# Kernel tuning notes

Hardware: AMD Instinct MI355X
Metric: run time of the kernel (lower is better)

## Reference

```python
import jax, jax.numpy as jnp
import numpy as np

B, M, N, I, O, NM = 16, 256, 256, 64, 64, 16


def setup_inputs() -> dict:
    key = jax.random.key(0)
    k1, k2, k3, k4, k5 = jax.random.split(key, 5)
    glorot = 1.0 / np.sqrt(I + O)
    return {
        "x": jax.random.normal(k1, (B, M, N, I), dtype=jnp.float32),
        "fw1": jax.random.normal(k2, (I, O, NM, NM, 2), dtype=jnp.float32) * glorot,
        "fw2": jax.random.normal(k3, (I, O, NM, NM, 2), dtype=jnp.float32) * glorot,
        "W": jax.random.normal(k4, (I, O), dtype=jnp.float32) * glorot,
        "b": jnp.zeros((O,), dtype=jnp.float32),
    }


def reference(x, fw1, fw2, W, b):
    # x: [B, M, N, I] -> [B, I, M, N]
    Bs, Ms, Ns, Is = x.shape
    nm = fw1.shape[2]
    xt = jnp.transpose(x, (0, 3, 1, 2))
    # forward rFFT over spatial dims, scaled by 1/sqrt(M*N) as in the TF code
    x_ft = jnp.fft.rfft2(xt, s=(Ms, Ns))  # [B, I, M, N//2+1] complex64
    x_ft = x_ft / jnp.asarray(np.sqrt(Ms * Ns), dtype=x_ft.dtype)
    # complex weights (stack-of-2 real/imag -> complex); complex einsum is
    # exactly the real/imag stacked matmul in the original
    w1 = jax.lax.complex(fw1[..., 0], fw1[..., 1])
    w2 = jax.lax.complex(fw2[..., 0], fw2[..., 1])
    top = jnp.einsum('bixy,ioxy->boxy', x_ft[:, :, :nm, :nm], w1)
    bot = jnp.einsum('bixy,ioxy->boxy', x_ft[:, :, -nm:, :nm], w2)
    mid = jnp.zeros((Bs, top.shape[1], Ms - 2 * nm, nm), dtype=top.dtype)
    out_ft = jnp.concatenate([top, mid, bot], axis=2)          # [B, O, M, nm]
    pad = jnp.zeros((Bs, top.shape[1], Ms, Ms // 2 + 1 - nm), dtype=top.dtype)
    out_ft = jnp.concatenate([out_ft, pad], axis=3)            # [B, O, M, M//2+1]
    y = jnp.fft.irfft2(out_ft, s=(Ns, Ms))                     # [B, O, N, M]
    # TF rescale: sqrt(prod of last two dims of out_ft) = sqrt(N*(M//2+1))
    y = y * jnp.asarray(np.sqrt(Ns * (Ms // 2 + 1)), dtype=y.dtype)
    y = jnp.transpose(y, (0, 2, 3, 1))                         # [B, M, N, O]
    return jax.nn.relu(y @ W + b + y)
```

## Files before the change

kernel.cpp:

```cpp
#include <hip/hip_runtime.h>
#include <hip/hip_bf16.h>


#define PI2F 6.283185307179586f

typedef __attribute__((ext_vector_type(8))) short short8v;
typedef __attribute__((ext_vector_type(4))) float f32x4;

static __device__ __forceinline__ unsigned short f_to_bf16(float f) {
  unsigned int u = __float_as_uint(f);
  u += 0x7fffu + ((u >> 16) & 1u);
  return (unsigned short)(u >> 16);
}
static __device__ __forceinline__ unsigned int pack_bf16(float lo, float hi) {
  return (unsigned int)f_to_bf16(lo) | ((unsigned int)f_to_bf16(hi) << 16);
}

__global__ __launch_bounds__(256) void k_prep(const float* __restrict__ fw1,
                                              const float* __restrict__ fw2,
                                              unsigned int* __restrict__ wTb,
                                              unsigned short* __restrict__ Eg,
                                              unsigned short* __restrict__ CSg,
                                              const float* __restrict__ Wg,
                                              unsigned short* __restrict__ Wtb) {
  int t = threadIdx.x;
  if (blockIdx.x == 256) {
    const float SC = 1.0f / 256.0f;
#pragma unroll
    for (int ky = 0; ky < 16; ++ky) {
      int idx = (ky * t) & 255;
      float ss, cc;
      sincosf(PI2F * (float)idx * (1.0f / 256.0f), &ss, &cc);
      Eg[(2 * ky) * 256 + t]     = f_to_bf16(cc * SC);
      Eg[(2 * ky + 1) * 256 + t] = f_to_bf16(-ss * SC);
      CSg[t * 32 + 2 * ky]       = f_to_bf16(cc);
      CSg[t * 32 + 2 * ky + 1]   = f_to_bf16(ss);
    }
#pragma unroll
    for (int k = 0; k < 16; ++k) {
      int p = k * 256 + t;
      Wtb[(p & 63) * 64 + (p >> 6)] = f_to_bf16(Wg[p]);
    }
    return;
  }
  int a  = blockIdx.x >> 3;
  int ic = blockIdx.x & 7;
  const float* w = (a < 16) ? fw1 : fw2;
  int xx = a & 15;
#pragma unroll
  for (int k = 0; k < 2; ++k) {
    int p = k * 256 + t;
    int i = ic * 8 + (p >> 6);
    int o = p & 63;
    const float4* s4 = reinterpret_cast<const float4*>(
        w + ((((size_t)i * 64 + o) * 16 + xx) * 16) * 2);
#pragma unroll
    for (int j = 0; j < 8; ++j) {
      float4 q = s4[j];
      wTb[(((size_t)(2 * j) * 32 + a) * 64 + i) * 64 + o]     = pack_bf16(q.x, q.y);
      wTb[(((size_t)(2 * j + 1) * 32 + a) * 64 + i) * 64 + o] = pack_bf16(q.z, q.w);
    }
  }
}

__global__ __launch_bounds__(256) void k1_mfma(const float* __restrict__ x,
                                               const unsigned short* __restrict__ Eg,
                                               unsigned int* __restrict__ Tb) {
  __shared__ __align__(16) unsigned short El[32 * 264];
  __shared__ __align__(16) float xs[2][2048];
  int bm = blockIdx.x;
  int b = bm >> 8, m = bm & 255;
  int tid = threadIdx.x;

  {
    const unsigned int* src = reinterpret_cast<const unsigned int*>(Eg);
    unsigned int* dst = reinterpret_cast<unsigned int*>(El);
#pragma unroll
    for (int t = 0; t < 16; ++t) {
      int idx = t * 256 + tid;
      dst[(idx >> 7) * 132 + (idx & 127)] = src[idx];
    }
  }

  const float* xrow = x + (size_t)bm * 16384;
  int lane = tid & 63, w = tid >> 6;
  int r16 = lane & 15, g4 = lane >> 4;

  int r0 = tid >> 4;
  int c4 = (tid & 15) * 4;
  int off0 = r0 * 64 + (c4 ^ (((r0 >> 3) & 3) << 4));
  int r1 = 16 + r0;
  int off1 = r1 * 64 + (c4 ^ (((r1 >> 3) & 3) << 4));
  int colr = (w * 16 + r16) ^ (g4 << 4);

  {
    const float4* s = reinterpret_cast<const float4*>(xrow);
    float4 v0 = s[tid], v1 = s[256 + tid];
    *reinterpret_cast<float4*>(&xs[0][off0]) = v0;
    *reinterpret_cast<float4*>(&xs[0][off1]) = v1;
  }
  __syncthreads();

  f32x4 z = {0.f, 0.f, 0.f, 0.f};
  f32x4 acc0 = z, acc1 = z;

#pragma unroll
  for (int c = 0; c < 8; ++c) {
    int cur = c & 1;
    if (c < 7) {
      const float4* s = reinterpret_cast<const float4*>(xrow + (c + 1) * 2048);
      float4 v0 = s[tid], v1 = s[256 + tid];
      *reinterpret_cast<float4*>(&xs[cur ^ 1][off0]) = v0;
      *reinterpret_cast<float4*>(&xs[cur ^ 1][off1]) = v1;
    }
    const float* xb = &xs[cur][g4 * 8 * 64 + colr];
    float xv[8];
#pragma unroll
    for (int j = 0; j < 8; ++j) xv[j] = xb[j * 64];
    short8v bfr;
#pragma unroll
    for (int j = 0; j < 8; ++j) bfr[j] = (short)f_to_bf16(xv[j]);
    int nb = c * 32 + g4 * 8;
    short8v a0 = *reinterpret_cast<const short8v*>(&El[r16 * 264 + nb]);
    short8v a1 = *reinterpret_cast<const short8v*>(&El[(16 + r16) * 264 + nb]);
    acc0 = __builtin_amdgcn_mfma_f32_16x16x32_bf16(a0, bfr, acc0, 0, 0, 0);
    acc1 = __builtin_amdgcn_mfma_f32_16x16x32_bf16(a1, bfr, acc1, 0, 0, 0);
    __syncthreads();
  }

  int i = w * 16 + r16;
#pragma unroll
  for (int mt = 0; mt < 2; ++mt) {
    f32x4 av = (mt == 0) ? acc0 : acc1;
    int ky_a = mt * 8 + g4 * 2;
    Tb[((size_t)(b * 16 + ky_a) * 256 + m) * 64 + i]     = pack_bf16(av[0], av[1]);
    Tb[((size_t)(b * 16 + ky_a + 1) * 256 + m) * 64 + i] = pack_bf16(av[2], av[3]);
  }
}

__global__ __launch_bounds__(1024) void k23_mix(const unsigned int* __restrict__ Tb,
                                                const unsigned int* __restrict__ wTb,
                                                float* __restrict__ OF) {
  __shared__ float Xpr[4][2048];
  __shared__ float Xpi[4][2048];
  int bky = blockIdx.x;
  int ky = bky & 15;
  int tid = threadIdx.x;

  int mc = tid >> 8, ih = tid & 15, ag = (tid >> 4) & 15;
  int m0 = mc * 64;
  const uint4* Tp4 = reinterpret_cast<const uint4*>(Tb) + (size_t)bky * 4096 + ih;

  float cd1, sd1n, cd2, sd2n;
  { float ss, cc; sincosf(PI2F * (float)ag * (1.0f / 256.0f), &ss, &cc); cd1 = cc; sd1n = -ss; }
  { float ss, cc; sincosf(PI2F * (float)(ag - 16) * (1.0f / 256.0f), &ss, &cc); cd2 = cc; sd2n = -ss; }
  float c1, s1, c2, s2;
  { int t = (ag * m0) & 255; float ss, cc; sincosf(PI2F * (float)t * (1.0f / 256.0f), &ss, &cc); c1 = cc; s1 = -ss; }
  { int t = ((ag + 240) * m0) & 255; float ss, cc; sincosf(PI2F * (float)t * (1.0f / 256.0f), &ss, &cc); c2 = cc; s2 = -ss; }

  float xr1[4], xi1[4], xr2[4], xi2[4];
#pragma unroll
  for (int ii = 0; ii < 4; ++ii) { xr1[ii] = xi1[ii] = xr2[ii] = xi2[ii] = 0.0f; }

#pragma unroll 4
  for (int m = 0; m < 64; ++m) {
    uint4 q = Tp4[(size_t)(m0 + m) * 16];
    unsigned int dv[4] = {q.x, q.y, q.z, q.w};
    float tre[4], tim[4];
#pragma unroll
    for (int ii = 0; ii < 4; ++ii) {
      tre[ii] = __uint_as_float(dv[ii] << 16);
      tim[ii] = __uint_as_float(dv[ii] & 0xffff0000u);
    }
#pragma unroll
    for (int ii = 0; ii < 4; ++ii) {
      xr1[ii] += tre[ii] * c1 - tim[ii] * s1;
      xi1[ii] += tre[ii] * s1 + tim[ii] * c1;
      xr2[ii] += tre[ii] * c2 - tim[ii] * s2;
      xi2[ii] += tre[ii] * s2 + tim[ii] * c2;
    }
    float cn;
    cn = c1 * cd1 - s1 * sd1n; s1 = c1 * sd1n + s1 * cd1; c1 = cn;
    cn = c2 * cd2 - s2 * sd2n; s2 = c2 * sd2n + s2 * cd2; c2 = cn;
  }
#pragma unroll
  for (int ii = 0; ii < 4; ++ii) {
    Xpr[mc][ag * 64 + ih * 4 + ii]        = xr1[ii];
    Xpi[mc][ag * 64 + ih * 4 + ii]        = xi1[ii];
    Xpr[mc][(ag + 16) * 64 + ih * 4 + ii] = xr2[ii];
    Xpi[mc][(ag + 16) * 64 + ih * 4 + ii] = xi2[ii];
  }
  __syncthreads();

#pragma unroll
  for (int j = 0; j < 2; ++j) {
    int s = j * 1024 + tid;
    Xpr[0][s] += Xpr[1][s] + Xpr[2][s] + Xpr[3][s];
    Xpi[0][s] += Xpi[1][s] + Xpi[2][s] + Xpi[3][s];
  }
  __syncthreads();

  int o = tid & 63, ab = tid >> 6;
#pragma unroll
  for (int half = 0; half < 2; ++half) {
    int a = ab + half * 16;
    const unsigned int* wp = wTb + (size_t)(ky * 32 + a) * 4096 + o;
    float ore = 0.0f, oim = 0.0f;
    for (int i = 0; i < 64; ++i) {
      float xr = Xpr[0][a * 64 + i];
      float xi = Xpi[0][a * 64 + i];
      unsigned int wv = wp[i * 64];
      float wr = __uint_as_float(wv << 16);
      float wi = __uint_as_float(wv & 0xffff0000u);
      ore += xr * wr - xi * wi;
      oim += xr * wi + xi * wr;
    }
    reinterpret_cast<float2*>(OF)[((size_t)bky * 32 + a) * 64 + o] =
        make_float2(ore, oim);
  }
}

__global__ __launch_bounds__(256) void k4_inv_kx(const float* __restrict__ OF,
                                                 uint4* __restrict__ Gb4) {
  int bx = blockIdx.x;
  int b = bx >> 6, ug = (bx >> 2) & 15, chunk = bx & 3;
  __shared__ float ct[256], st[256];
  {
    float ssv, ccv;
    sincosf(PI2F * (float)threadIdx.x * (1.0f / 256.0f), &ssv, &ccv);
    ct[threadIdx.x] = ccv;
    st[threadIdx.x] = ssv;
  }
  __syncthreads();

  int o = threadIdx.x & 63, us = threadIdx.x >> 6;
  int u0 = ug * 16 + us * 4;
  const float SC2 = 0.002772904280510622f;
  const float2* OFb = reinterpret_cast<const float2*>(OF) +
                      ((size_t)b * 16 + chunk * 4) * 2048;

  float accr[4][4], acci[4][4];
#pragma unroll
  for (int du = 0; du < 4; ++du)
#pragma unroll
    for (int kyl = 0; kyl < 4; ++kyl) { accr[du][kyl] = 0.0f; acci[du][kyl] = 0.0f; }

  for (int a = 0; a < 32; ++a) {
    int kx = (a < 16) ? a : (224 + a);
    float ofr[4], ofi[4];
#pragma unroll
    for (int kyl = 0; kyl < 4; ++kyl) {
      float2 v = OFb[(kyl * 32 + a) * 64 + o];
      ofr[kyl] = v.x; ofi[kyl] = v.y;
    }
#pragma unroll
    for (int du = 0; du < 4; ++du) {
      int t = (kx * (u0 + du)) & 255;
      float cv = ct[t], sv = st[t];
#pragma unroll
      for (int kyl = 0; kyl < 4; ++kyl) {
        accr[du][kyl] += ofr[kyl] * cv - ofi[kyl] * sv;
        acci[du][kyl] += ofr[kyl] * sv + ofi[kyl] * cv;
      }
    }
  }
#pragma unroll
  for (int du = 0; du < 4; ++du) {
    int u = u0 + du;
    unsigned int wv[4];
#pragma unroll
    for (int kyl = 0; kyl < 4; ++kyl) {
      int ky = chunk * 4 + kyl;
      float sc = SC2 * ((ky == 0) ? 1.0f : 2.0f);
      wv[kyl] = pack_bf16(accr[du][kyl] * sc, -acci[du][kyl] * sc);
    }
    uint4 pk; pk.x = wv[0]; pk.y = wv[1]; pk.z = wv[2]; pk.w = wv[3];
    Gb4[(((size_t)b * 256 + u) * 4 + chunk) * 64 + o] = pk;
  }
}

__global__ __launch_bounds__(256) void k5_mfma(const unsigned short* __restrict__ Gb,
                                               const unsigned short* __restrict__ CSg,
                                               const unsigned short* __restrict__ Wtb,
                                               const float* __restrict__ bias,
                                               float* __restrict__ out) {
  __shared__ __align__(16) unsigned short yl[256 * 72];

  int blk = blockIdx.x;
  int tid = threadIdx.x;
  int lane = tid & 63, w = tid >> 6;
  int r16 = lane & 15, g4 = lane >> 4;
  int kc0 = g4 * 8;

  f32x4 z = {0.f, 0.f, 0.f, 0.f};
  f32x4 acc[4][4];

  short8v af[4], bfx[4];
#pragma unroll
  for (int vt = 0; vt < 4; ++vt)
    af[vt] = *reinterpret_cast<const short8v*>(&CSg[(w * 64 + vt * 16 + r16) * 32 + kc0]);
#pragma unroll
  for (int ot = 0; ot < 4; ++ot)
    bfx[ot] = *reinterpret_cast<const short8v*>(
        &Gb[(((size_t)blk * 4 + g4) * 64 + ot * 16 + r16) * 8]);
#pragma unroll
  for (int vt = 0; vt < 4; ++vt)
#pragma unroll
    for (int ot = 0; ot < 4; ++ot)
      acc[vt][ot] = __builtin_amdgcn_mfma_f32_16x16x32_bf16(af[vt], bfx[ot], z, 0, 0, 0);

#pragma unroll
  for (int vt = 0; vt < 4; ++vt)
#pragma unroll
    for (int ot = 0; ot < 4; ++ot)
#pragma unroll
      for (int r = 0; r < 4; ++r)
        yl[(w * 64 + vt * 16 + g4 * 4 + r) * 72 + ot * 16 + r16] = f_to_bf16(acc[vt][ot][r]);

#pragma unroll
  for (int ot = 0; ot < 4; ++ot) {
    float bv = bias[ot * 16 + r16];
#pragma unroll
    for (int vt = 0; vt < 4; ++vt)
#pragma unroll
      for (int r = 0; r < 4; ++r) acc[vt][ot][r] += bv;
  }

#pragma unroll
  for (int ks = 0; ks < 2; ++ks) {
    int k0 = ks * 32 + kc0;
    short8v ya[4], wb[4];
#pragma unroll
    for (int vt = 0; vt < 4; ++vt)
      ya[vt] = *reinterpret_cast<const short8v*>(&yl[(w * 64 + vt * 16 + r16) * 72 + k0]);
#pragma unroll
    for (int ot = 0; ot < 4; ++ot)
      wb[ot] = *reinterpret_cast<const short8v*>(&Wtb[(ot * 16 + r16) * 64 + k0]);
#pragma unroll
    for (int vt = 0; vt < 4; ++vt)
#pragma unroll
      for (int ot = 0; ot < 4; ++ot)
        acc[vt][ot] = __builtin_amdgcn_mfma_f32_16x16x32_bf16(ya[vt], wb[ot], acc[vt][ot], 0, 0, 0);
  }

  float* ob = out + (size_t)blk * 16384;
  float* tw = reinterpret_cast<float*>(&yl[w * 4608]);
#pragma unroll
  for (int vt = 0; vt < 4; ++vt) {
#pragma unroll
    for (int ot = 0; ot < 4; ++ot)
#pragma unroll
      for (int r = 0; r < 4; ++r)
        tw[(g4 * 4 + r) * 68 + ot * 16 + r16] = fmaxf(acc[vt][ot][r], 0.0f);
    float* obase = ob + (size_t)(w * 64 + vt * 16) * 64;
#pragma unroll
    for (int q = 0; q < 4; ++q) {
      float4 vv = *reinterpret_cast<const float4*>(
          &tw[(q * 4 + (lane >> 4)) * 68 + (lane & 15) * 4]);
      *reinterpret_cast<float4*>(&obase[q * 256 + lane * 4]) = vv;
    }
  }
}

extern "C" void kernel_launch(void* const* d_in, const int* in_sizes, int n_in,
                              void* d_out, int out_size, void* d_ws, size_t ws_size,
                              hipStream_t stream) {
  const float* x   = (const float*)d_in[0];
  const float* fw1 = (const float*)d_in[1];
  const float* fw2 = (const float*)d_in[2];
  const float* W   = (const float*)d_in[3];
  const float* bb  = (const float*)d_in[4];
  float* out = (float*)d_out;

  float* ws = (float*)d_ws;
  unsigned int* wTb  = (unsigned int*)ws;
  unsigned int* Tb   = (unsigned int*)(ws + 2097152);
  float* OF          = ws + 6291456;
  unsigned int* Gb   = (unsigned int*)(ws + 7340032);
  unsigned short* Eg  = (unsigned short*)(ws + 11534336);
  unsigned short* CSg = Eg + 8192;
  unsigned short* Wtb = CSg + 8192;

  hipLaunchKernelGGL(k_prep,   dim3(257),  dim3(256),  0, stream,
                     fw1, fw2, wTb, Eg, CSg, W, Wtb);
  hipLaunchKernelGGL(k1_mfma,  dim3(4096), dim3(256),  0, stream, x, Eg, Tb);
  hipLaunchKernelGGL(k23_mix,  dim3(256),  dim3(1024), 0, stream, Tb, wTb, OF);
  hipLaunchKernelGGL(k4_inv_kx,dim3(1024), dim3(256),  0, stream, OF, (uint4*)Gb);
  hipLaunchKernelGGL(k5_mfma,  dim3(4096), dim3(256),  0, stream,
                     (const unsigned short*)Gb, CSg, Wtb, bb, out);
}
```

Baseline: 209.9 us.

## Fuse inverse kx DFT into the spectral mixing kernel and relayout Gb

Folds the inverse DFT along kx (formerly k4_inv_kx) into the mixing kernel, so the mixed spectrum stays in shared memory and never goes through the OF buffer. It also drops one launch. Gb is now laid out per (b, ky) with u and o as inner dimensions, and k5 gathers its B fragments with strided 32-bit loads instead of one 16-byte vector load. The trade-off is that the fused stage runs on only 256 blocks and recomputes twiddles per (u, a), while k5's loads are less coalesced.

Result: slower. 228.0 us (+8.6%).

```diff
diff --git a/kernel.cpp b/kernel.cpp
--- a/kernel.cpp
+++ b/kernel.cpp
@@ -138,14 +138,22 @@
   }
 }
 
-__global__ __launch_bounds__(1024) void k23_mix(const unsigned int* __restrict__ Tb,
-                                                const unsigned int* __restrict__ wTb,
-                                                float* __restrict__ OF) {
+__global__ __launch_bounds__(1024) void k23g(const unsigned int* __restrict__ Tb,
+                                             const unsigned int* __restrict__ wTb,
+                                             unsigned int* __restrict__ Gb) {
   __shared__ float Xpr[4][2048];
   __shared__ float Xpi[4][2048];
+  __shared__ float ct[256], st[256];
   int bky = blockIdx.x;
   int ky = bky & 15;
   int tid = threadIdx.x;
+
+  if (tid < 256) {
+    float ssv, ccv;
+    sincosf(PI2F * (float)tid * (1.0f / 256.0f), &ssv, &ccv);
+    ct[tid] = ccv;
+    st[tid] = ssv;
+  }
 
   int mc = tid >> 8, ih = tid & 15, ag = (tid >> 4) & 15;
   int m0 = mc * 64;
@@ -192,11 +200,19 @@
   }
   __syncthreads();
 
+  float red_r[2], red_i[2];
 #pragma unroll
   for (int j = 0; j < 2; ++j) {
     int s = j * 1024 + tid;
-    Xpr[0][s] += Xpr[1][s] + Xpr[2][s] + Xpr[3][s];
-    Xpi[0][s] += Xpi[1][s] + Xpi[2][s] + Xpi[3][s];
+    red_r[j] = Xpr[0][s] + Xpr[1][s] + Xpr[2][s] + Xpr[3][s];
+    red_i[j] = Xpi[0][s] + Xpi[1][s] + Xpi[2][s] + Xpi[3][s];
+  }
+  __syncthreads();
+#pragma unroll
+  for (int j = 0; j < 2; ++j) {
+    int s = j * 1024 + tid;
+    Xpr[0][s] = red_r[j];
+    Xpi[0][s] = red_i[j];
   }
   __syncthreads();
 
@@ -215,71 +231,34 @@
       ore += xr * wr - xi * wi;
       oim += xr * wi + xi * wr;
     }
-    reinterpret_cast<float2*>(OF)[((size_t)bky * 32 + a) * 64 + o] =
-        make_float2(ore, oim);
-  }
-}
-
-__global__ __launch_bounds__(256) void k4_inv_kx(const float* __restrict__ OF,
-                                                 uint4* __restrict__ Gb4) {
-  int bx = blockIdx.x;
-  int b = bx >> 6, ug = (bx >> 2) & 15, chunk = bx & 3;
-  __shared__ float ct[256], st[256];
+    Xpr[1][a * 64 + o] = ore;
+    Xpi[1][a * 64 + o] = oim;
+  }
+  __syncthreads();
+
   {
-    float ssv, ccv;
-    sincosf(PI2F * (float)threadIdx.x * (1.0f / 256.0f), &ssv, &ccv);
-    ct[threadIdx.x] = ccv;
-    st[threadIdx.x] = ssv;
-  }
-  __syncthreads();
-
-  int o = threadIdx.x & 63, us = threadIdx.x >> 6;
-  int u0 = ug * 16 + us * 4;
-  const float SC2 = 0.002772904280510622f;
-  const float2* OFb = reinterpret_cast<const float2*>(OF) +
-                      ((size_t)b * 16 + chunk * 4) * 2048;
-
-  float accr[4][4], acci[4][4];
-#pragma unroll
-  for (int du = 0; du < 4; ++du)
-#pragma unroll
-    for (int kyl = 0; kyl < 4; ++kyl) { accr[du][kyl] = 0.0f; acci[du][kyl] = 0.0f; }
-
-  for (int a = 0; a < 32; ++a) {
-    int kx = (a < 16) ? a : (224 + a);
-    float ofr[4], ofi[4];
-#pragma unroll
-    for (int kyl = 0; kyl < 4; ++kyl) {
-      float2 v = OFb[(kyl * 32 + a) * 64 + o];
-      ofr[kyl] = v.x; ofi[kyl] = v.y;
-    }
-#pragma unroll
-    for (int du = 0; du < 4; ++du) {
-      int t = (kx * (u0 + du)) & 255;
-      float cv = ct[t], sv = st[t];
-#pragma unroll
-      for (int kyl = 0; kyl < 4; ++kyl) {
-        accr[du][kyl] += ofr[kyl] * cv - ofi[kyl] * sv;
-        acci[du][kyl] += ofr[kyl] * sv + ofi[kyl] * cv;
+    const float sc = 0.002772904280510622f * ((ky == 0) ? 1.0f : 2.0f);
+    unsigned int* Gp = Gb + (size_t)bky * 16384 + o;
+#pragma unroll 2
+    for (int j = 0; j < 16; ++j) {
+      int u = ab * 16 + j;
+      float accr = 0.0f, acci = 0.0f;
+#pragma unroll 8
+      for (int a = 0; a < 32; ++a) {
+        int kx = (a < 16) ? a : (224 + a);
+        int t = (kx * u) & 255;
+        float cv = ct[t], sv = st[t];
+        float ofr = Xpr[1][a * 64 + o];
+        float ofi = Xpi[1][a * 64 + o];
+        accr += ofr * cv - ofi * sv;
+        acci += ofr * sv + ofi * cv;
       }
-    }
-  }
-#pragma unroll
-  for (int du = 0; du < 4; ++du) {
-    int u = u0 + du;
-    unsigned int wv[4];
-#pragma unroll
-    for (int kyl = 0; kyl < 4; ++kyl) {
-      int ky = chunk * 4 + kyl;
-      float sc = SC2 * ((ky == 0) ? 1.0f : 2.0f);
-      wv[kyl] = pack_bf16(accr[du][kyl] * sc, -acci[du][kyl] * sc);
-    }
-    uint4 pk; pk.x = wv[0]; pk.y = wv[1]; pk.z = wv[2]; pk.w = wv[3];
-    Gb4[(((size_t)b * 256 + u) * 4 + chunk) * 64 + o] = pk;
-  }
-}
-
-__global__ __launch_bounds__(256) void k5_mfma(const unsigned short* __restrict__ Gb,
+      Gp[(size_t)u * 64] = pack_bf16(accr * sc, -acci * sc);
+    }
+  }
+}
+
+__global__ __launch_bounds__(256) void k5_mfma(const unsigned int* __restrict__ Gb,
                                                const unsigned short* __restrict__ CSg,
                                                const unsigned short* __restrict__ Wtb,
                                                const float* __restrict__ bias,
@@ -295,14 +274,20 @@
   f32x4 z = {0.f, 0.f, 0.f, 0.f};
   f32x4 acc[4][4];
 
+  int b = blk >> 8, u = blk & 255;
+  const unsigned int* Gp = Gb + (size_t)b * 262144 + (size_t)u * 64;
   short8v af[4], bfx[4];
 #pragma unroll
   for (int vt = 0; vt < 4; ++vt)
     af[vt] = *reinterpret_cast<const short8v*>(&CSg[(w * 64 + vt * 16 + r16) * 32 + kc0]);
 #pragma unroll
-  for (int ot = 0; ot < 4; ++ot)
-    bfx[ot] = *reinterpret_cast<const short8v*>(
-        &Gb[(((size_t)blk * 4 + g4) * 64 + ot * 16 + r16) * 8]);
+  for (int ot = 0; ot < 4; ++ot) {
+    union { short8v s; unsigned int d[4]; } bu;
+#pragma unroll
+    for (int q = 0; q < 4; ++q)
+      bu.d[q] = Gp[(size_t)(g4 * 4 + q) * 16384 + ot * 16 + r16];
+    bfx[ot] = bu.s;
+  }
 #pragma unroll
   for (int vt = 0; vt < 4; ++vt)
 #pragma unroll
@@ -375,17 +360,15 @@
   float* ws = (float*)d_ws;
   unsigned int* wTb  = (unsigned int*)ws;
   unsigned int* Tb   = (unsigned int*)(ws + 2097152);
-  float* OF          = ws + 6291456;
-  unsigned int* Gb   = (unsigned int*)(ws + 7340032);
-  unsigned short* Eg  = (unsigned short*)(ws + 11534336);
+  unsigned int* Gb   = (unsigned int*)(ws + 6291456);
+  unsigned short* Eg  = (unsigned short*)(ws + 10485760);
   unsigned short* CSg = Eg + 8192;
   unsigned short* Wtb = CSg + 8192;
 
   hipLaunchKernelGGL(k_prep,   dim3(257),  dim3(256),  0, stream,
                      fw1, fw2, wTb, Eg, CSg, W, Wtb);
   hipLaunchKernelGGL(k1_mfma,  dim3(4096), dim3(256),  0, stream, x, Eg, Tb);
-  hipLaunchKernelGGL(k23_mix,  dim3(256),  dim3(1024), 0, stream, Tb, wTb, OF);
-  hipLaunchKernelGGL(k4_inv_kx,dim3(1024), dim3(256),  0, stream, OF, (uint4*)Gb);
+  hipLaunchKernelGGL(k23g,     dim3(256),  dim3(1024), 0, stream, Tb, wTb, Gb);
   hipLaunchKernelGGL(k5_mfma,  dim3(4096), dim3(256),  0, stream,
-                     (const unsigned short*)Gb, CSg, Wtb, bb, out);
-}
+                     Gb, CSg, Wtb, bb, out);
+}
```
